# Kernel tuning notes

Hardware: AMD Instinct MI355X
Metric: run time of the kernel (lower is better)

Reference implementation:

```python
import jax, jax.numpy as jnp
import numpy as np

TEMPERATURE = 11.313708498984761  # sqrt(d_k) with d_k=128
RELU15_CAP = 15.0


def setup_inputs() -> dict:
    key = jax.random.key(0)
    kq, kk, kv = jax.random.split(key, 3)
    B, H, S, D = 4, 16, 1024, 128
    q = jax.random.normal(kq, (B, H, S, D), dtype=jnp.float32)
    k = jax.random.normal(kk, (B, H, S, D), dtype=jnp.float32)
    v = jax.random.normal(kv, (B, H, S, D), dtype=jnp.float32)
    mask = jnp.ones((B, 1, S, S), dtype=jnp.int32)  # broadcast over heads
    return {"q": q, "k": k, "v": v, "mask": mask}


def reference(q, k, v, mask):
    # attn = (q / temperature) @ k^T  -> [B,H,Sq,Sk]
    attn = jnp.einsum("bhqd,bhkd->bhqk", q / TEMPERATURE, k)
    # masked_fill(mask == 0, -1e9)
    attn = jnp.where(mask == 0, jnp.float32(-1e9), attn)
    # ReLU15 activation (custom softmax replacement): clamp to [0, 15]
    attn = jnp.clip(attn, 0.0, RELU15_CAP)
    # dropout with p=0.0 is identity (inference reference)
    out = jnp.einsum("bhqk,bhkd->bhqd", attn, v)
    return (out, attn)
```

## Files before the change

### kernel.cpp

```cpp
#include <hip/hip_runtime.h>
#include <stdint.h>

#define B_   4
#define H_   16
#define S_   1024
#define D_   128
#define BM   64
#define BN   32
#define NKT  (S_ / BN)
#define NTHREADS 256

typedef float f32x4 __attribute__((ext_vector_type(4)));
typedef short s16x8 __attribute__((ext_vector_type(8)));
typedef short s16x4 __attribute__((ext_vector_type(4)));

static __device__ __forceinline__ uint16_t f2bf(float f) {
  uint32_t u = __float_as_uint(f);
  u += 0x7FFFu + ((u >> 16) & 1u);
  return (uint16_t)(u >> 16);
}
static __device__ __forceinline__ float bf2f(uint16_t h) {
  return __uint_as_float((uint32_t)h << 16);
}

static __device__ __forceinline__ void gl16(const void* g, void* l) {
  __builtin_amdgcn_global_load_lds(
      (const __attribute__((address_space(1))) unsigned int*)g,
      (__attribute__((address_space(3))) unsigned int*)l, 16, 0, 0);
}

#define WSK_BYTES  16777216
#define WSV_BYTES  16777216
#define WSM_BYTES  524288
#define WS_NEED    (WSK_BYTES + WSV_BYTES + WSM_BYTES)

__global__ __launch_bounds__(256)
void prepass_kernel(const float* __restrict__ k, const float* __restrict__ v,
                    const int* __restrict__ mask,
                    char* __restrict__ wsK, char* __restrict__ wsV,
                    uint32_t* __restrict__ wsM)
{
  int gid = blockIdx.x * 256 + threadIdx.x;
  if (gid < 1048576) {
    int tile = gid >> 9, c = gid & 511;
    int ks = c >> 7, nt = (c >> 6) & 1, lane = c & 63;
    int row = (tile & 31) * 32 + 16 * nt + (lane & 15);
    int col = 32 * ks + 8 * (lane >> 4);
    const float* src = k + ((size_t)(tile >> 5) * S_ + row) * D_ + col;
    f32x4 x0 = *(const f32x4*)src;
    f32x4 x1 = *(const f32x4*)(src + 4);
    s16x8 h;
    h[0]=f2bf(x0[0]); h[1]=f2bf(x0[1]); h[2]=f2bf(x0[2]); h[3]=f2bf(x0[3]);
    h[4]=f2bf(x1[0]); h[5]=f2bf(x1[1]); h[6]=f2bf(x1[2]); h[7]=f2bf(x1[3]);
    *(s16x8*)(wsK + (size_t)gid * 16) = h;
  } else if (gid < 2097152) {
    int gv = gid - 1048576;
    int tile = gv >> 9, c = gv & 511;
    int nt = c >> 6, lane = c & 63;
    int d   = 16 * nt + (lane & 15);
    int kv0 = (tile & 31) * 32 + 8 * (lane >> 4);
    const float* src = v + ((size_t)(tile >> 5) * S_ + kv0) * D_ + d;
    s16x8 h;
    #pragma unroll
    for (int i = 0; i < 8; ++i) h[i] = f2bf(src[(size_t)i * D_]);
    *(s16x8*)(wsV + (size_t)gv * 16) = h;
  } else if (gid < 2228224) {
    int gm = gid - 2097152;
    const int* src = mask + (size_t)(gm >> 5) * S_ + (gm & 31) * 32;
    uint32_t bits = 0;
    #pragma unroll
    for (int i = 0; i < 32; ++i) bits |= (src[i] != 0 ? 1u : 0u) << i;
    wsM[gm] = bits;
  }
}

__global__ __launch_bounds__(NTHREADS)
__attribute__((amdgpu_waves_per_eu(4, 4)))
void attn_relu15_main(const float* __restrict__ q,
                      const char* __restrict__ wsK, const char* __restrict__ wsV,
                      const uint32_t* __restrict__ wsM,
                      float* __restrict__ outp, float* __restrict__ attnp)
{
  const int blk = blockIdx.x;
  const int g   = (blk & 7) * 128 + (blk >> 3);
  const int bh  = g >> 4;
  const int qt  = g & 15;
  const int b   = bh >> 4;

  const int tid  = threadIdx.x;
  const int lane = tid & 63;
  const int wq   = tid >> 6;
  const int lhi  = lane >> 4;
  const int llo  = lane & 15;

  __shared__ __align__(16) char smem[36864];
  char* const lK0 = smem;
  char* const lV0 = smem + 16384;
  char* const lS  = smem + 32768 + wq * 1024;

  const float*    qg = q + (size_t)bh * (S_ * D_) + (size_t)qt * BM * D_;
  const char*     kw = wsK + (size_t)(bh * 32) * 8192;
  const char*     vw = wsV + (size_t)(bh * 32) * 8192;
  const uint32_t* mw0 = wsM + ((size_t)b * S_ + qt * BM + 16 * wq) * 32;
  float*          ag = attnp + (size_t)bh * S_ * S_ + (size_t)qt * BM * S_;
  float*          og = outp  + (size_t)bh * (S_ * D_) + (size_t)qt * BM * D_;

  const float invT = 0.08838834764831843f;

  s16x8 qf[4];
  {
    const float* qrow = qg + (size_t)(16 * wq + llo) * D_;
    #pragma unroll
    for (int ks = 0; ks < 4; ++ks) {
      int d0 = 32 * ks + 8 * lhi;
      f32x4 x0 = *(const f32x4*)(qrow + d0);
      f32x4 x1 = *(const f32x4*)(qrow + d0 + 4);
      s16x8 h;
      h[0]=f2bf(x0[0]*invT); h[1]=f2bf(x0[1]*invT); h[2]=f2bf(x0[2]*invT); h[3]=f2bf(x0[3]*invT);
      h[4]=f2bf(x1[0]*invT); h[5]=f2bf(x1[1]*invT); h[6]=f2bf(x1[2]*invT); h[7]=f2bf(x1[3]*invT);
      qf[ks] = h;
    }
  }

  #pragma unroll
  for (int rep = 0; rep < 2; ++rep) {
    gl16(kw + rep * 4096 + tid * 16, lK0 + rep * 4096 + wq * 1024);
    gl16(vw + rep * 4096 + tid * 16, lV0 + rep * 4096 + wq * 1024);
  }
  asm volatile("s_waitcnt vmcnt(0) lgkmcnt(0)" ::: "memory");
  __builtin_amdgcn_s_barrier();
  __builtin_amdgcn_sched_barrier(0);

  f32x4 oacc[8];
  #pragma unroll
  for (int i = 0; i < 8; ++i) oacc[i] = (f32x4){0.f,0.f,0.f,0.f};

  int cur = 0;
  for (int kt = 0; kt < NKT; ++kt) {
    const bool pf = (kt + 1 < NKT);
    char* lKc = lK0 + cur * 8192;
    char* lVc = lV0 + cur * 8192;

    uint32_t mwv[4];
    #pragma unroll
    for (int j = 0; j < 4; ++j)
      mwv[j] = mw0[(size_t)(4 * lhi + j) * 32 + kt];

    if (pf) {
      const char* kn = kw + (size_t)(kt + 1) * 8192;
      const char* vn = vw + (size_t)(kt + 1) * 8192;
      char* lKn = lK0 + (cur ^ 1) * 8192;
      char* lVn = lV0 + (cur ^ 1) * 8192;
      #pragma unroll
      for (int rep = 0; rep < 2; ++rep) {
        gl16(kn + rep * 4096 + tid * 16, lKn + rep * 4096 + wq * 1024);
        gl16(vn + rep * 4096 + tid * 16, lVn + rep * 4096 + wq * 1024);
      }
    }
    __builtin_amdgcn_sched_barrier(0);

    f32x4 sacc[2];
    sacc[0] = (f32x4){0.f,0.f,0.f,0.f}; sacc[1] = sacc[0];
    #pragma unroll
    for (int ks = 0; ks < 4; ++ks) {
      s16x8 bfr[2];
      #pragma unroll
      for (int nt = 0; nt < 2; ++nt)
        bfr[nt] = *(s16x8*)(lKc + (ks * 2 + nt) * 1024 + lane * 16);
      #pragma unroll
      for (int nt = 0; nt < 2; ++nt)
        sacc[nt] = __builtin_amdgcn_mfma_f32_16x16x32_bf16(qf[ks], bfr[nt], sacc[nt], 0, 0, 0);
    }

    #pragma unroll
    for (int nt = 0; nt < 2; ++nt) {
      char* sb = lS + (2 * nt + (llo >> 3)) * 256 + (llo & 7) * 2;
      #pragma unroll
      for (int j = 0; j < 4; ++j) {
        float val = fminf(fmaxf(sacc[nt][j], 0.f), 15.f);
        if (!((mwv[j] >> (16 * nt + llo)) & 1u)) val = 0.f;
        *(uint16_t*)(sb + (4 * lhi + j) * 16) = f2bf(val);
      }
    }

    #pragma unroll
    for (int p = 0; p < 2; ++p) {
      int r  = 16 * wq + p * 8 + (lane >> 3);
      int cb = lane & 7;
      s16x4 sv = *(s16x4*)(lS + (cb >> 1) * 256 + ((r & 15) * 16) + (cb & 1) * 8);
      f32x4 a;
      a[0]=bf2f((uint16_t)sv[0]); a[1]=bf2f((uint16_t)sv[1]);
      a[2]=bf2f((uint16_t)sv[2]); a[3]=bf2f((uint16_t)sv[3]);
      __builtin_nontemporal_store(a, (f32x4*)(ag + (size_t)r * S_ + kt * BN + cb * 4));
    }

    {
      s16x8 saf = *(s16x8*)(lS + lane * 16);
      #pragma unroll
      for (int nt = 0; nt < 8; ++nt) {
        s16x8 vb = *(s16x8*)(lVc + nt * 1024 + lane * 16);
        oacc[nt] = __builtin_amdgcn_mfma_f32_16x16x32_bf16(saf, vb, oacc[nt], 0, 0, 0);
      }
    }

    asm volatile("s_waitcnt vmcnt(2) lgkmcnt(0)" ::: "memory");
    __builtin_amdgcn_s_barrier();
    __builtin_amdgcn_sched_barrier(0);
    cur ^= 1;
  }

  #pragma unroll
  for (int nt = 0; nt < 8; ++nt) {
    int n = 16 * nt + llo;
    #pragma unroll
    for (int j = 0; j < 4; ++j) {
      int m = 16 * wq + 4 * lhi + j;
      __builtin_nontemporal_store(oacc[nt][j], og + (size_t)m * D_ + n);
    }
  }
}

#define LDS_BARRIER() do {                                   \
    asm volatile("s_waitcnt lgkmcnt(0)" ::: "memory");       \
    __builtin_amdgcn_s_barrier();                            \
    __builtin_amdgcn_sched_barrier(0);                       \
  } while (0)

__global__ __launch_bounds__(NTHREADS)
__attribute__((amdgpu_waves_per_eu(4, 4)))
void attn_relu15_fallback(const float* __restrict__ q, const float* __restrict__ k,
                          const float* __restrict__ v, const int* __restrict__ mask,
                          float* __restrict__ outp, float* __restrict__ attnp)
{
  const int blk = blockIdx.x;
  const int g   = (blk & 7) * 128 + (blk >> 3);
  const int bh  = g >> 4;
  const int qt  = g & 15;
  const int b   = bh >> 4;
  const int tid  = threadIdx.x;
  const int lane = tid & 63;
  const int wq   = tid >> 6;
  const int lhi  = lane >> 4;
  const int llo  = lane & 15;

  __shared__ __align__(16) char smem[36864];
  char* const lK0 = smem;
  char* const lV0 = smem + 16384;
  char* const lS  = smem + 32768 + wq * 1024;

  const float* qg = q + (size_t)bh * (S_ * D_) + (size_t)qt * BM * D_;
  const float* kg = k + (size_t)bh * (S_ * D_);
  const float* vg = v + (size_t)bh * (S_ * D_);
  const int*   mg = mask  + (size_t)b * S_ * S_ + (size_t)qt * BM * S_;
  float*       ag = attnp + (size_t)bh * S_ * S_ + (size_t)qt * BM * S_;
  float*       og = outp  + (size_t)bh * (S_ * D_) + (size_t)qt * BM * D_;
  const float invT = 0.08838834764831843f;

  #define K_O(rep)   ((tid + NTHREADS * (rep)) * 8)
  #define K_ROW(o)   ((((o) >> 10) & 1) * 16 + (((o) >> 4) & 15))
  #define K_COL(o)   (((o) >> 11) * 32 + (((o) >> 8) & 3) * 8 + (((o) >> 3) & 1) * 4)

  s16x8 qf[4];
  {
    const float* qrow = qg + (size_t)(16 * wq + llo) * D_;
    #pragma unroll
    for (int ks = 0; ks < 4; ++ks) {
      int d0 = 32 * ks + 8 * lhi;
      f32x4 x0 = *(const f32x4*)(qrow + d0);
      f32x4 x1 = *(const f32x4*)(qrow + d0 + 4);
      s16x8 h;
      h[0]=f2bf(x0[0]*invT); h[1]=f2bf(x0[1]*invT); h[2]=f2bf(x0[2]*invT); h[3]=f2bf(x0[3]*invT);
      h[4]=f2bf(x1[0]*invT); h[5]=f2bf(x1[1]*invT); h[6]=f2bf(x1[2]*invT); h[7]=f2bf(x1[3]*invT);
      qf[ks] = h;
    }
  }
  {
    #pragma unroll
    for (int rep = 0; rep < 4; ++rep) {
      int o = K_O(rep);
      f32x4 x = *(const f32x4*)(kg + K_ROW(o) * D_ + K_COL(o));
      s16x4 h; h[0]=f2bf(x[0]); h[1]=f2bf(x[1]); h[2]=f2bf(x[2]); h[3]=f2bf(x[3]);
      *(s16x4*)(lK0 + o) = h;
    }
    #pragma unroll
    for (int rep = 0; rep < 4; ++rep) {
      int bid = (tid >> 2) + 64 * rep;
      int kb = bid >> 5, db = bid & 31, l2 = lane & 3;
      f32x4 x = *(const f32x4*)(vg + (size_t)(kb * 4 + l2) * D_ + db * 4);
      float v0=x[0], v1=x[1], v2=x[2], v3=x[3], t;
      t=(l2&1)?v0:v1; t=__shfl_xor(t,1); if(l2&1)v0=t; else v1=t;
      t=(l2&1)?v2:v3; t=__shfl_xor(t,1); if(l2&1)v2=t; else v3=t;
      t=(l2&2)?v0:v2; t=__shfl_xor(t,2); if(l2&2)v0=t; else v2=t;
      t=(l2&2)?v1:v3; t=__shfl_xor(t,2); if(l2&2)v1=t; else v3=t;
      int dd = db * 4 + l2;
      s16x4 h; h[0]=f2bf(v0); h[1]=f2bf(v1); h[2]=f2bf(v2); h[3]=f2bf(v3);
      *(s16x4*)(lV0 + (dd >> 4) * 1024 + ((kb >> 1) & 3) * 256
                    + (dd & 15) * 16 + (kb & 1) * 8) = h;
    }
  }
  LDS_BARRIER();

  f32x4 oacc[8];
  #pragma unroll
  for (int i = 0; i < 8; ++i) oacc[i] = (f32x4){0.f,0.f,0.f,0.f};

  int cur = 0;
  for (int kt = 0; kt < NKT; ++kt) {
    const bool pf = (kt + 1 < NKT);
    char* lKc = lK0 + cur * 8192;
    char* lVc = lV0 + cur * 8192;
    f32x4 kst[4];
    const float* kgt = kg + (size_t)(kt + 1) * BN * D_;
    if (pf) {
      #pragma unroll
      for (int rep = 0; rep < 4; ++rep) {
        int o = K_O(rep);
        kst[rep] = *(const f32x4*)(kgt + K_ROW(o) * D_ + K_COL(o));
      }
    }
    int mreg[8];
    #pragma unroll
    for (int nt = 0; nt < 2; ++nt)
      #pragma unroll
      for (int j = 0; j < 4; ++j)
        mreg[nt * 4 + j] =
          mg[(size_t)(16 * wq + 4 * lhi + j) * S_ + kt * BN + 16 * nt + llo];

    f32x4 sacc[2];
    sacc[0] = (f32x4){0.f,0.f,0.f,0.f}; sacc[1] = sacc[0];
    #pragma unroll
    for (int ks = 0; ks < 4; ++ks) {
      s16x8 bfr[2];
      #pragma unroll
      for (int nt = 0; nt < 2; ++nt)
        bfr[nt] = *(s16x8*)(lKc + (ks * 2 + nt) * 1024 + lane * 16);
      #pragma unroll
      for (int nt = 0; nt < 2; ++nt)
        sacc[nt] = __builtin_amdgcn_mfma_f32_16x16x32_bf16(qf[ks], bfr[nt], sacc[nt], 0, 0, 0);
    }

    f32x4 vst[4];
    const float* vgt = vg + (size_t)(kt + 1) * BN * D_;
    if (pf) {
      char* lKn = lK0 + (cur ^ 1) * 8192;
      #pragma unroll
      for (int rep = 0; rep < 4; ++rep) {
        f32x4 x = kst[rep];
        s16x4 h; h[0]=f2bf(x[0]); h[1]=f2bf(x[1]); h[2]=f2bf(x[2]); h[3]=f2bf(x[3]);
        *(s16x4*)(lKn + K_O(rep)) = h;
      }
      #pragma unroll
      for (int rep = 0; rep < 4; ++rep) {
        int bid = (tid >> 2) + 64 * rep;
        int kb = bid >> 5, db = bid & 31, l2 = lane & 3;
        vst[rep] = *(const f32x4*)(vgt + (size_t)(kb * 4 + l2) * D_ + db * 4);
      }
    }

    #pragma unroll
    for (int nt = 0; nt < 2; ++nt) {
      char* sb = lS + (2 * nt + (llo >> 3)) * 256 + (llo & 7) * 2;
      #pragma unroll
      for (int j = 0; j < 4; ++j) {
        float val = fminf(fmaxf(sacc[nt][j], 0.f), 15.f);
        if (mreg[nt * 4 + j] == 0) val = 0.f;
        *(uint16_t*)(sb + (4 * lhi + j) * 16) = f2bf(val);
      }
    }
    {
      s16x8 saf = *(s16x8*)(lS + lane * 16);
      #pragma unroll
      for (int nt = 0; nt < 8; ++nt) {
        s16x8 vb = *(s16x8*)(lVc + nt * 1024 + lane * 16);
        oacc[nt] = __builtin_amdgcn_mfma_f32_16x16x32_bf16(saf, vb, oacc[nt], 0, 0, 0);
      }
    }
    #pragma unroll
    for (int p = 0; p < 2; ++p) {
      int r  = 16 * wq + p * 8 + (lane >> 3);
      int cb = lane & 7;
      s16x4 sv = *(s16x4*)(lS + (cb >> 1) * 256 + ((r & 15) * 16) + (cb & 1) * 8);
      f32x4 a;
      a[0]=bf2f((uint16_t)sv[0]); a[1]=bf2f((uint16_t)sv[1]);
      a[2]=bf2f((uint16_t)sv[2]); a[3]=bf2f((uint16_t)sv[3]);
      __builtin_nontemporal_store(a, (f32x4*)(ag + (size_t)r * S_ + kt * BN + cb * 4));
    }
    if (pf) {
      char* lVn = lV0 + (cur ^ 1) * 8192;
      #pragma unroll
      for (int rep = 0; rep < 4; ++rep) {
        int bid = (tid >> 2) + 64 * rep;
        int kb = bid >> 5, db = bid & 31, l2 = lane & 3;
        f32x4 x = vst[rep];
        float v0=x[0], v1=x[1], v2=x[2], v3=x[3], t;
        t=(l2&1)?v0:v1; t=__shfl_xor(t,1); if(l2&1)v0=t; else v1=t;
        t=(l2&1)?v2:v3; t=__shfl_xor(t,1); if(l2&1)v2=t; else v3=t;
        t=(l2&2)?v0:v2; t=__shfl_xor(t,2); if(l2&2)v0=t; else v2=t;
        t=(l2&2)?v1:v3; t=__shfl_xor(t,2); if(l2&2)v1=t; else v3=t;
        int dd = db * 4 + l2;
        s16x4 h; h[0]=f2bf(v0); h[1]=f2bf(v1); h[2]=f2bf(v2); h[3]=f2bf(v3);
        *(s16x4*)(lVn + (dd >> 4) * 1024 + ((kb >> 1) & 3) * 256
                      + (dd & 15) * 16 + (kb & 1) * 8) = h;
      }
    }
    LDS_BARRIER();
    cur ^= 1;
  }
  #pragma unroll
  for (int nt = 0; nt < 8; ++nt) {
    int n = 16 * nt + llo;
    #pragma unroll
    for (int j = 0; j < 4; ++j) {
      int m = 16 * wq + 4 * lhi + j;
      __builtin_nontemporal_store(oacc[nt][j], og + (size_t)m * D_ + n);
    }
  }
}

extern "C" void kernel_launch(void* const* d_in, const int* in_sizes, int n_in,
                              void* d_out, int out_size, void* d_ws, size_t ws_size,
                              hipStream_t stream) {
  const float* q    = (const float*)d_in[0];
  const float* k    = (const float*)d_in[1];
  const float* v    = (const float*)d_in[2];
  const int*   mask = (const int*)d_in[3];
  float* outp  = (float*)d_out;
  float* attnp = outp + (size_t)B_ * H_ * S_ * D_;

  if (ws_size >= (size_t)WS_NEED && d_ws != nullptr) {
    char*     wsK = (char*)d_ws;
    char*     wsV = wsK + WSK_BYTES;
    uint32_t* wsM = (uint32_t*)(wsK + WSK_BYTES + WSV_BYTES);
    prepass_kernel<<<8704, 256, 0, stream>>>(k, v, mask, wsK, wsV, wsM);
    attn_relu15_main<<<dim3(B_ * H_ * (S_ / BM)), NTHREADS, 0, stream>>>(
        q, wsK, wsV, wsM, outp, attnp);
  } else {
    attn_relu15_fallback<<<dim3(B_ * H_ * (S_ / BM)), NTHREADS, 0, stream>>>(
        q, k, v, mask, outp, attnp);
  }
}
```

Before: 101.5 us.

## Double query tile per block to reuse K/V tiles across two row groups

Raises the query tile from 64 to 128 rows so each wave handles two 16-row groups, reusing each K/V fragment loaded from LDS for twice as many MFMAs. It halves the number of blocks and the total K/V traffic, relaxes the occupancy hint to two waves per EU, and transposes the mask bitmap layout so a wave reads its mask words with one vector load per row group. The attention tile is now read back from LDS once and used both for the output store and as the PV operand, replacing a separate re-read. The cost is higher register pressure, fewer blocks in flight to hide latency, and a larger LDS footprint.

```diff
diff --git a/kernel.cpp b/kernel.cpp
--- a/kernel.cpp
+++ b/kernel.cpp
@@ -5,7 +5,7 @@
 #define H_   16
 #define S_   1024
 #define D_   128
-#define BM   64
+#define BM   128
 #define BN   32
 #define NKT  (S_ / BN)
 #define NTHREADS 256
@@ -13,6 +13,7 @@
 typedef float f32x4 __attribute__((ext_vector_type(4)));
 typedef short s16x8 __attribute__((ext_vector_type(8)));
 typedef short s16x4 __attribute__((ext_vector_type(4)));
+typedef int   i32x4 __attribute__((ext_vector_type(4)));
 
 static __device__ __forceinline__ uint16_t f2bf(float f) {
   uint32_t u = __float_as_uint(f);
@@ -66,25 +67,27 @@
     *(s16x8*)(wsV + (size_t)gv * 16) = h;
   } else if (gid < 2228224) {
     int gm = gid - 2097152;
-    const int* src = mask + (size_t)(gm >> 5) * S_ + (gm & 31) * 32;
+    int gro = gm >> 5;
+    int w   = gm & 31;
+    const int* src = mask + (size_t)gro * S_ + w * 32;
     uint32_t bits = 0;
     #pragma unroll
     for (int i = 0; i < 32; ++i) bits |= (src[i] != 0 ? 1u : 0u) << i;
-    wsM[gm] = bits;
+    wsM[((size_t)(gro >> 10) * 32 + w) * 1024 + (gro & 1023)] = bits;
   }
 }
 
 __global__ __launch_bounds__(NTHREADS)
-__attribute__((amdgpu_waves_per_eu(4, 4)))
+__attribute__((amdgpu_waves_per_eu(2)))
 void attn_relu15_main(const float* __restrict__ q,
                       const char* __restrict__ wsK, const char* __restrict__ wsV,
                       const uint32_t* __restrict__ wsM,
                       float* __restrict__ outp, float* __restrict__ attnp)
 {
   const int blk = blockIdx.x;
-  const int g   = (blk & 7) * 128 + (blk >> 3);
-  const int bh  = g >> 4;
-  const int qt  = g & 15;
+  const int g   = (blk & 7) * 64 + (blk >> 3);
+  const int bh  = g >> 3;
+  const int qt  = g & 7;
   const int b   = bh >> 4;
 
   const int tid  = threadIdx.x;
@@ -93,23 +96,24 @@
   const int lhi  = lane >> 4;
   const int llo  = lane & 15;
 
-  __shared__ __align__(16) char smem[36864];
+  __shared__ __align__(16) char smem[40960];
   char* const lK0 = smem;
   char* const lV0 = smem + 16384;
-  char* const lS  = smem + 32768 + wq * 1024;
-
-  const float*    qg = q + (size_t)bh * (S_ * D_) + (size_t)qt * BM * D_;
-  const char*     kw = wsK + (size_t)(bh * 32) * 8192;
-  const char*     vw = wsV + (size_t)(bh * 32) * 8192;
-  const uint32_t* mw0 = wsM + ((size_t)b * S_ + qt * BM + 16 * wq) * 32;
-  float*          ag = attnp + (size_t)bh * S_ * S_ + (size_t)qt * BM * S_;
-  float*          og = outp  + (size_t)bh * (S_ * D_) + (size_t)qt * BM * D_;
+  char* const lSw = smem + 32768 + wq * 2048;
+
+  const float*    qg  = q + (size_t)bh * (S_ * D_) + (size_t)qt * BM * D_;
+  const char*     kw  = wsK + (size_t)(bh * 32) * 8192;
+  const char*     vw  = wsV + (size_t)(bh * 32) * 8192;
+  const uint32_t* mwb = wsM + (size_t)b * 32768 + qt * BM + 32 * wq + 4 * lhi;
+  float*          ag  = attnp + (size_t)bh * S_ * S_ + (size_t)qt * BM * S_;
+  float*          og  = outp  + (size_t)bh * (S_ * D_) + (size_t)qt * BM * D_;
 
   const float invT = 0.08838834764831843f;
 
-  s16x8 qf[4];
-  {
-    const float* qrow = qg + (size_t)(16 * wq + llo) * D_;
+  s16x8 qf[2][4];
+  #pragma unroll
+  for (int qb = 0; qb < 2; ++qb) {
+    const float* qrow = qg + (size_t)(32 * wq + 16 * qb + llo) * D_;
     #pragma unroll
     for (int ks = 0; ks < 4; ++ks) {
       int d0 = 32 * ks + 8 * lhi;
@@ -118,7 +122,7 @@
       s16x8 h;
       h[0]=f2bf(x0[0]*invT); h[1]=f2bf(x0[1]*invT); h[2]=f2bf(x0[2]*invT); h[3]=f2bf(x0[3]*invT);
       h[4]=f2bf(x1[0]*invT); h[5]=f2bf(x1[1]*invT); h[6]=f2bf(x1[2]*invT); h[7]=f2bf(x1[3]*invT);
-      qf[ks] = h;
+      qf[qb][ks] = h;
     }
   }
 
@@ -131,9 +135,11 @@
   __builtin_amdgcn_s_barrier();
   __builtin_amdgcn_sched_barrier(0);
 
-  f32x4 oacc[8];
-  #pragma unroll
-  for (int i = 0; i < 8; ++i) oacc[i] = (f32x4){0.f,0.f,0.f,0.f};
+  f32x4 oacc[2][8];
+  #pragma unroll
+  for (int i = 0; i < 2; ++i)
+    #pragma unroll
+    for (int j = 0; j < 8; ++j) oacc[i][j] = (f32x4){0.f,0.f,0.f,0.f};
 
   int cur = 0;
   for (int kt = 0; kt < NKT; ++kt) {
@@ -141,10 +147,10 @@
     char* lKc = lK0 + cur * 8192;
     char* lVc = lV0 + cur * 8192;
 
-    uint32_t mwv[4];
-    #pragma unroll
-    for (int j = 0; j < 4; ++j)
-      mwv[j] = mw0[(size_t)(4 * lhi + j) * 32 + kt];
+    i32x4 mv[2];
+    #pragma unroll
+    for (int qb = 0; qb < 2; ++qb)
+      mv[qb] = *(const i32x4*)(mwb + (size_t)kt * 1024 + 16 * qb);
 
     if (pf) {
       const char* kn = kw + (size_t)(kt + 1) * 8192;
@@ -159,8 +165,9 @@
     }
     __builtin_amdgcn_sched_barrier(0);
 
-    f32x4 sacc[2];
-    sacc[0] = (f32x4){0.f,0.f,0.f,0.f}; sacc[1] = sacc[0];
+    f32x4 sacc[2][2];
+    #pragma unroll
+    for (int i = 0; i < 2; ++i) { sacc[i][0] = (f32x4){0,0,0,0}; sacc[i][1] = sacc[i][0]; }
     #pragma unroll
     for (int ks = 0; ks < 4; ++ks) {
       s16x8 bfr[2];
@@ -168,56 +175,69 @@
       for (int nt = 0; nt < 2; ++nt)
         bfr[nt] = *(s16x8*)(lKc + (ks * 2 + nt) * 1024 + lane * 16);
       #pragma unroll
-      for (int nt = 0; nt < 2; ++nt)
-        sacc[nt] = __builtin_amdgcn_mfma_f32_16x16x32_bf16(qf[ks], bfr[nt], sacc[nt], 0, 0, 0);
-    }
-
-    #pragma unroll
-    for (int nt = 0; nt < 2; ++nt) {
-      char* sb = lS + (2 * nt + (llo >> 3)) * 256 + (llo & 7) * 2;
-      #pragma unroll
-      for (int j = 0; j < 4; ++j) {
-        float val = fminf(fmaxf(sacc[nt][j], 0.f), 15.f);
-        if (!((mwv[j] >> (16 * nt + llo)) & 1u)) val = 0.f;
-        *(uint16_t*)(sb + (4 * lhi + j) * 16) = f2bf(val);
-      }
-    }
-
-    #pragma unroll
-    for (int p = 0; p < 2; ++p) {
-      int r  = 16 * wq + p * 8 + (lane >> 3);
-      int cb = lane & 7;
-      s16x4 sv = *(s16x4*)(lS + (cb >> 1) * 256 + ((r & 15) * 16) + (cb & 1) * 8);
-      f32x4 a;
-      a[0]=bf2f((uint16_t)sv[0]); a[1]=bf2f((uint16_t)sv[1]);
-      a[2]=bf2f((uint16_t)sv[2]); a[3]=bf2f((uint16_t)sv[3]);
-      __builtin_nontemporal_store(a, (f32x4*)(ag + (size_t)r * S_ + kt * BN + cb * 4));
-    }
-
-    {
-      s16x8 saf = *(s16x8*)(lS + lane * 16);
-      #pragma unroll
-      for (int nt = 0; nt < 8; ++nt) {
-        s16x8 vb = *(s16x8*)(lVc + nt * 1024 + lane * 16);
-        oacc[nt] = __builtin_amdgcn_mfma_f32_16x16x32_bf16(saf, vb, oacc[nt], 0, 0, 0);
-      }
-    }
-
-    asm volatile("s_waitcnt vmcnt(2) lgkmcnt(0)" ::: "memory");
+      for (int qb = 0; qb < 2; ++qb)
+        #pragma unroll
+        for (int nt = 0; nt < 2; ++nt)
+          sacc[qb][nt] = __builtin_amdgcn_mfma_f32_16x16x32_bf16(
+              qf[qb][ks], bfr[nt], sacc[qb][nt], 0, 0, 0);
+    }
+
+    #pragma unroll
+    for (int qb = 0; qb < 2; ++qb) {
+      #pragma unroll
+      for (int nt = 0; nt < 2; ++nt) {
+        char* sb = lSw + qb * 1024 + (2 * nt + (llo >> 3)) * 256 + (llo & 7) * 2;
+        #pragma unroll
+        for (int j = 0; j < 4; ++j) {
+          float val = fminf(fmaxf(sacc[qb][nt][j], 0.f), 15.f);
+          if (!(((uint32_t)mv[qb][j] >> (16 * nt + llo)) & 1u)) val = 0.f;
+          *(uint16_t*)(sb + (4 * lhi + j) * 16) = f2bf(val);
+        }
+      }
+    }
+
+    s16x8 pa[2];
+    #pragma unroll
+    for (int qb = 0; qb < 2; ++qb)
+      pa[qb] = *(s16x8*)(lSw + qb * 1024 + lane * 16);
+
+    #pragma unroll
+    for (int qb = 0; qb < 2; ++qb) {
+      float* dst = ag + (size_t)(32 * wq + 16 * qb + llo) * S_ + kt * BN + 8 * lhi;
+      f32x4 a0, a1;
+      #pragma unroll
+      for (int i = 0; i < 4; ++i) {
+        a0[i] = bf2f((uint16_t)pa[qb][i]);
+        a1[i] = bf2f((uint16_t)pa[qb][4 + i]);
+      }
+      __builtin_nontemporal_store(a0, (f32x4*)dst);
+      __builtin_nontemporal_store(a1, (f32x4*)(dst + 4));
+    }
+
+    #pragma unroll
+    for (int nt = 0; nt < 8; ++nt) {
+      s16x8 vb = *(s16x8*)(lVc + nt * 1024 + lane * 16);
+      #pragma unroll
+      for (int qb = 0; qb < 2; ++qb)
+        oacc[qb][nt] = __builtin_amdgcn_mfma_f32_16x16x32_bf16(
+            pa[qb], vb, oacc[qb][nt], 0, 0, 0);
+    }
+
+    asm volatile("s_waitcnt vmcnt(4) lgkmcnt(0)" ::: "memory");
     __builtin_amdgcn_s_barrier();
     __builtin_amdgcn_sched_barrier(0);
     cur ^= 1;
   }
 
   #pragma unroll
-  for (int nt = 0; nt < 8; ++nt) {
-    int n = 16 * nt + llo;
+  for (int qb = 0; qb < 2; ++qb)
     #pragma unroll
     for (int j = 0; j < 4; ++j) {
-      int m = 16 * wq + 4 * lhi + j;
-      __builtin_nontemporal_store(oacc[nt][j], og + (size_t)m * D_ + n);
-    }
-  }
+      int m = 32 * wq + 16 * qb + 4 * lhi + j;
+      #pragma unroll
+      for (int nt = 0; nt < 8; ++nt)
+        __builtin_nontemporal_store(oacc[qb][nt][j], og + (size_t)m * D_ + 16 * nt + llo);
+    }
 }
 
 #define LDS_BARRIER() do {                                   \
@@ -248,12 +268,12 @@
   char* const lV0 = smem + 16384;
   char* const lS  = smem + 32768 + wq * 1024;
 
-  const float* qg = q + (size_t)bh * (S_ * D_) + (size_t)qt * BM * D_;
+  const float* qg = q + (size_t)bh * (S_ * D_) + (size_t)qt * 64 * D_;
   const float* kg = k + (size_t)bh * (S_ * D_);
   const float* vg = v + (size_t)bh * (S_ * D_);
-  const int*   mg = mask  + (size_t)b * S_ * S_ + (size_t)qt * BM * S_;
-  float*       ag = attnp + (size_t)bh * S_ * S_ + (size_t)qt * BM * S_;
-  float*       og = outp  + (size_t)bh * (S_ * D_) + (size_t)qt * BM * D_;
+  const int*   mg = mask  + (size_t)b * S_ * S_ + (size_t)qt * 64 * S_;
+  float*       ag = attnp + (size_t)bh * S_ * S_ + (size_t)qt * 64 * S_;
+  float*       og = outp  + (size_t)bh * (S_ * D_) + (size_t)qt * 64 * D_;
   const float invT = 0.08838834764831843f;
 
   #define K_O(rep)   ((tid + NTHREADS * (rep)) * 8)
@@ -435,7 +455,7 @@
     attn_relu15_main<<<dim3(B_ * H_ * (S_ / BM)), NTHREADS, 0, stream>>>(
         q, wsK, wsV, wsM, outp, attnp);
   } else {
-    attn_relu15_fallback<<<dim3(B_ * H_ * (S_ / BM)), NTHREADS, 0, stream>>>(
+    attn_relu15_fallback<<<dim3(B_ * H_ * (S_ / 64)), NTHREADS, 0, stream>>>(
         q, k, v, mask, outp, attnp);
   }
 }
```

Result: slower. 175.9 us (median of 2 runs) (+73.3%).

## Swap MFMA operands so P stays in registers, relayout V and mask

Applied to the files above, without the earlier changes.

The QK^T MFMA now takes K as the A operand and Q as the B operand, so each lane's accumulator already holds the P fragment the PV MFMA needs. That removes the LDS round trip before the second matmul. The V prepass reorders its k-rows and the mask bitmask is transposed to a [b][kt][row] layout, letting each lane fetch one mask word per tile instead of four. The LDS staging for the attn output gains padded rows (72-byte stride) to reduce bank conflicts. The cost is a slightly larger shared buffer and the need for the permuted V layout to exactly match the new P lane mapping.

```diff
diff --git a/kernel.cpp b/kernel.cpp
--- a/kernel.cpp
+++ b/kernel.cpp
@@ -57,20 +57,23 @@
     int gv = gid - 1048576;
     int tile = gv >> 9, c = gv & 511;
     int nt = c >> 6, lane = c & 63;
-    int d   = 16 * nt + (lane & 15);
-    int kv0 = (tile & 31) * 32 + 8 * (lane >> 4);
-    const float* src = v + ((size_t)(tile >> 5) * S_ + kv0) * D_ + d;
+    int llo = lane & 15, lhi = lane >> 4;
+    int d   = 16 * nt + llo;
+    const float* src = v + ((size_t)(tile >> 5) * S_ + (tile & 31) * 32 + 4 * lhi) * D_ + d;
     s16x8 h;
     #pragma unroll
-    for (int i = 0; i < 8; ++i) h[i] = f2bf(src[(size_t)i * D_]);
+    for (int p = 0; p < 8; ++p)
+      h[p] = f2bf(src[(size_t)((p & 3) + 16 * (p >> 2)) * D_]);
     *(s16x8*)(wsV + (size_t)gv * 16) = h;
   } else if (gid < 2228224) {
     int gm = gid - 2097152;
-    const int* src = mask + (size_t)(gm >> 5) * S_ + (gm & 31) * 32;
+    int gro = gm >> 5;
+    int w   = gm & 31;
+    const int* src = mask + (size_t)gro * S_ + w * 32;
     uint32_t bits = 0;
     #pragma unroll
     for (int i = 0; i < 32; ++i) bits |= (src[i] != 0 ? 1u : 0u) << i;
-    wsM[gm] = bits;
+    wsM[((size_t)(gro >> 10) * 32 + w) * 1024 + (gro & 1023)] = bits;
   }
 }
 
@@ -93,17 +96,17 @@
   const int lhi  = lane >> 4;
   const int llo  = lane & 15;
 
-  __shared__ __align__(16) char smem[36864];
+  __shared__ __align__(16) char smem[37376];
   char* const lK0 = smem;
   char* const lV0 = smem + 16384;
-  char* const lS  = smem + 32768 + wq * 1024;
-
-  const float*    qg = q + (size_t)bh * (S_ * D_) + (size_t)qt * BM * D_;
-  const char*     kw = wsK + (size_t)(bh * 32) * 8192;
-  const char*     vw = wsV + (size_t)(bh * 32) * 8192;
-  const uint32_t* mw0 = wsM + ((size_t)b * S_ + qt * BM + 16 * wq) * 32;
-  float*          ag = attnp + (size_t)bh * S_ * S_ + (size_t)qt * BM * S_;
-  float*          og = outp  + (size_t)bh * (S_ * D_) + (size_t)qt * BM * D_;
+  char* const lS  = smem + 32768 + wq * 1152;
+
+  const float*    qg  = q + (size_t)bh * (S_ * D_) + (size_t)qt * BM * D_;
+  const char*     kw  = wsK + (size_t)(bh * 32) * 8192;
+  const char*     vw  = wsV + (size_t)(bh * 32) * 8192;
+  const uint32_t* mwb = wsM + (size_t)b * 32768 + qt * BM + 16 * wq + llo;
+  float*          ag  = attnp + (size_t)bh * S_ * S_ + (size_t)qt * BM * S_;
+  float*          og  = outp  + (size_t)bh * (S_ * D_) + (size_t)qt * BM * D_;
 
   const float invT = 0.08838834764831843f;
 
@@ -141,10 +144,8 @@
     char* lKc = lK0 + cur * 8192;
     char* lVc = lV0 + cur * 8192;
 
-    uint32_t mwv[4];
-    #pragma unroll
-    for (int j = 0; j < 4; ++j)
-      mwv[j] = mw0[(size_t)(4 * lhi + j) * 32 + kt];
+    uint32_t mword = mwb[(size_t)kt * 1024];
+    __builtin_amdgcn_sched_barrier(0);
 
     if (pf) {
       const char* kn = kw + (size_t)(kt + 1) * 8192;
@@ -169,38 +170,39 @@
         bfr[nt] = *(s16x8*)(lKc + (ks * 2 + nt) * 1024 + lane * 16);
       #pragma unroll
       for (int nt = 0; nt < 2; ++nt)
-        sacc[nt] = __builtin_amdgcn_mfma_f32_16x16x32_bf16(qf[ks], bfr[nt], sacc[nt], 0, 0, 0);
-    }
-
+        sacc[nt] = __builtin_amdgcn_mfma_f32_16x16x32_bf16(bfr[nt], qf[ks], sacc[nt], 0, 0, 0);
+    }
+
+    s16x8 pa;
     #pragma unroll
     for (int nt = 0; nt < 2; ++nt) {
-      char* sb = lS + (2 * nt + (llo >> 3)) * 256 + (llo & 7) * 2;
       #pragma unroll
       for (int j = 0; j < 4; ++j) {
         float val = fminf(fmaxf(sacc[nt][j], 0.f), 15.f);
-        if (!((mwv[j] >> (16 * nt + llo)) & 1u)) val = 0.f;
-        *(uint16_t*)(sb + (4 * lhi + j) * 16) = f2bf(val);
-      }
+        if (!((mword >> (16 * nt + 4 * lhi + j)) & 1u)) val = 0.f;
+        pa[nt * 4 + j] = (short)f2bf(val);
+      }
+      s16x4 h4 = { pa[nt*4], pa[nt*4+1], pa[nt*4+2], pa[nt*4+3] };
+      *(s16x4*)(lS + llo * 72 + nt * 32 + lhi * 8) = h4;
+    }
+
+    #pragma unroll
+    for (int nt = 0; nt < 8; ++nt) {
+      s16x8 vb = *(s16x8*)(lVc + nt * 1024 + lane * 16);
+      oacc[nt] = __builtin_amdgcn_mfma_f32_16x16x32_bf16(pa, vb, oacc[nt], 0, 0, 0);
     }
 
     #pragma unroll
     for (int p = 0; p < 2; ++p) {
-      int r  = 16 * wq + p * 8 + (lane >> 3);
-      int cb = lane & 7;
-      s16x4 sv = *(s16x4*)(lS + (cb >> 1) * 256 + ((r & 15) * 16) + (cb & 1) * 8);
+      int rq   = lane >> 3;
+      int part = lane & 7;
+      int r    = 8 * p + rq;
+      s16x4 sv = *(s16x4*)(lS + r * 72 + part * 8);
       f32x4 a;
       a[0]=bf2f((uint16_t)sv[0]); a[1]=bf2f((uint16_t)sv[1]);
       a[2]=bf2f((uint16_t)sv[2]); a[3]=bf2f((uint16_t)sv[3]);
-      __builtin_nontemporal_store(a, (f32x4*)(ag + (size_t)r * S_ + kt * BN + cb * 4));
-    }
-
-    {
-      s16x8 saf = *(s16x8*)(lS + lane * 16);
-      #pragma unroll
-      for (int nt = 0; nt < 8; ++nt) {
-        s16x8 vb = *(s16x8*)(lVc + nt * 1024 + lane * 16);
-        oacc[nt] = __builtin_amdgcn_mfma_f32_16x16x32_bf16(saf, vb, oacc[nt], 0, 0, 0);
-      }
+      __builtin_nontemporal_store(a,
+          (f32x4*)(ag + (size_t)(16 * wq + r) * S_ + kt * BN + part * 4));
     }
 
     asm volatile("s_waitcnt vmcnt(2) lgkmcnt(0)" ::: "memory");
@@ -248,12 +250,12 @@
   char* const lV0 = smem + 16384;
   char* const lS  = smem + 32768 + wq * 1024;
 
-  const float* qg = q + (size_t)bh * (S_ * D_) + (size_t)qt * BM * D_;
+  const float* qg = q + (size_t)bh * (S_ * D_) + (size_t)qt * 64 * D_;
   const float* kg = k + (size_t)bh * (S_ * D_);
   const float* vg = v + (size_t)bh * (S_ * D_);
-  const int*   mg = mask  + (size_t)b * S_ * S_ + (size_t)qt * BM * S_;
-  float*       ag = attnp + (size_t)bh * S_ * S_ + (size_t)qt * BM * S_;
-  float*       og = outp  + (size_t)bh * (S_ * D_) + (size_t)qt * BM * D_;
+  const int*   mg = mask  + (size_t)b * S_ * S_ + (size_t)qt * 64 * S_;
+  float*       ag = attnp + (size_t)bh * S_ * S_ + (size_t)qt * 64 * S_;
+  float*       og = outp  + (size_t)bh * (S_ * D_) + (size_t)qt * 64 * D_;
   const float invT = 0.08838834764831843f;
 
   #define K_O(rep)   ((tid + NTHREADS * (rep)) * 8)
@@ -435,7 +437,7 @@
     attn_relu15_main<<<dim3(B_ * H_ * (S_ / BM)), NTHREADS, 0, stream>>>(
         q, wsK, wsV, wsM, outp, attnp);
   } else {
-    attn_relu15_fallback<<<dim3(B_ * H_ * (S_ / BM)), NTHREADS, 0, stream>>>(
+    attn_relu15_fallback<<<dim3(B_ * H_ * (S_ / 64)), NTHREADS, 0, stream>>>(
         q, k, v, mask, outp, attnp);
   }
 }
```

Measured after the change: 104.6 us. 3.0% more time.
